# Optimization experiments

Hardware: AMD Instinct MI355X
Metric: run time of the kernel (lower is better)

The kernel has to match this reference:

```python
import jax, jax.numpy as jnp
import numpy as np

B, T, D = 4, 4096, 1024
EPS = 1e-5  # FusedRMSNormSwishGate default eps


def setup_inputs() -> dict:
    key = jax.random.key(0)
    ks = jax.random.split(key, 6)
    s = 1.0 / np.sqrt(D)
    return {
        "x": jax.random.normal(ks[0], (B, T, D), jnp.float32),
        "Wi": jax.random.normal(ks[1], (D, D), jnp.float32) * s,
        "Wf": jax.random.normal(ks[2], (D, D), jnp.float32) * s,
        "Wg": jax.random.normal(ks[3], (D, D), jnp.float32) * s,
        "Wo": jax.random.normal(ks[4], (D, D), jnp.float32) * s,
        "norm_w": jnp.ones((D,), jnp.float32),
    }


def _hgrn_scan(f, i):
    # h_t = f_t * h_{t-1} + i_t  (elementwise gated linear recurrence)
    # associative combine: (f1,i1) o (f2,i2) = (f1*f2, i1*f2 + i2)
    def combine(a, b):
        fa, ia = a
        fb, ib = b
        return fa * fb, ia * fb + ib

    _, h = jax.lax.associative_scan(combine, (f, i), axis=1)
    return h


def reference(x, Wi, Wf, Wg, Wo, norm_w):
    # projections
    i = x @ Wi.T                                  # [B,T,D]
    f = jax.nn.sigmoid(x @ Wf.T)                  # forget gate in (0,1)
    # swiglu(i, 1-f): silu on the value, gated by the input gate (1-f)
    inp = jax.nn.silu(i) * (1.0 - f)
    # hierarchically-gated linear recurrence (chunk/parallel scan form)
    h = _hgrn_scan(f, inp)                        # [B,T,D]
    # RMSNorm(h) * swish(g) output gate
    g = x @ Wg.T
    rms = h * jax.lax.rsqrt(jnp.mean(h * h, axis=-1, keepdims=True) + EPS)
    o = (rms * norm_w) * (g * jax.nn.sigmoid(g))
    return o @ Wo.T
```

## Files before the change

kernel.cpp:

```cpp
#include <hip/hip_runtime.h>
#include <hip/hip_bf16.h>

typedef unsigned short u16;
using bf16x8 = __bf16 __attribute__((ext_vector_type(8)));
using u16x8  = unsigned short __attribute__((ext_vector_type(8)));
using f32x4  = float  __attribute__((ext_vector_type(4)));

#define BB 4
#define TT 4096
#define DD 1024
#define MROWS (BB*TT)
#define CT 64
#define NC (TT/CT)

__device__ __forceinline__ float sigm(float x) { return 1.0f / (1.0f + __expf(-x)); }
__device__ __forceinline__ u16 f2bf(float f) {
    __hip_bfloat16 h = __float2bfloat16(f);
    return *reinterpret_cast<u16*>(&h);
}
__device__ __forceinline__ float bf2f(u16 u) { return __uint_as_float(((unsigned)u) << 16); }

__device__ __forceinline__ void async_cp16(const u16* g, u16* l) {
    __builtin_amdgcn_global_load_lds(
        (const __attribute__((address_space(1))) unsigned int*)g,
        (__attribute__((address_space(3))) unsigned int*)l, 16, 0, 0);
}

__global__ __launch_bounds__(256) void conv_w4_kernel(const float* __restrict__ w0,
                                                      const float* __restrict__ w1,
                                                      const float* __restrict__ w2,
                                                      const float* __restrict__ w3,
                                                      u16* __restrict__ dst) {
    int i = blockIdx.x * 256 + threadIdx.x;
    int sel = i >> 18;
    int off = i & 262143;
    const float* s = (sel == 0) ? w0 : (sel == 1) ? w1 : (sel == 2) ? w2 : w3;
    float4 v = *(const float4*)(s + (size_t)off * 4);
    ushort4 u;
    u.x = f2bf(v.x); u.y = f2bf(v.y); u.z = f2bf(v.z); u.w = f2bf(v.w);
    *(ushort4*)(dst + ((size_t)sel << 20) + (size_t)off * 4) = u;
}

#define BM 128
#define BN 128
#define BK 64

template <typename AT, typename OutT>
__global__ __launch_bounds__(256, 2)
void gemm_bt(const AT* __restrict__ Ag, const u16* __restrict__ Bg, int K,
             OutT* __restrict__ P0, OutT* __restrict__ P1, OutT* __restrict__ P2) {
    __shared__ u16 As[BM * BK];
    __shared__ u16 Bs[BN * BK];

    const int tid  = threadIdx.x;
    const int lane = tid & 63;
    const int wid  = tid >> 6;
    const int wm   = wid >> 1;
    const int wn   = wid & 1;
    const int lr   = lane & 15;
    const int lq   = lane >> 4;

    const long bM  = (long)blockIdx.y * BM;
    const long bN0 = (long)blockIdx.x * BN;

    const f32x4 zero = {0.f, 0.f, 0.f, 0.f};
    f32x4 acc[4][4];
#pragma unroll
    for (int i = 0; i < 4; i++)
#pragma unroll
        for (int j = 0; j < 4; j++) acc[i][j] = zero;

    for (int kt = 0; kt < K; kt += BK) {
        float4 afr[4][2];
        if constexpr (sizeof(AT) == 4) {
#pragma unroll
            for (int j = 0; j < 4; j++) {
                const int G  = j * 256 + tid;
                const int m  = G >> 3;
                const int gk = (G & 7) ^ (m & 7);
                const float* s = (const float*)Ag + (bM + m) * (long)K + kt + gk * 8;
                afr[j][0] = *(const float4*)s;
                afr[j][1] = *(const float4*)(s + 4);
            }
        }
        __syncthreads();
#pragma unroll
        for (int j = 0; j < 4; j++) {
            const int G  = j * 256 + tid;
            const int m  = G >> 3;
            const int gk = (G & 7) ^ (m & 7);
            if constexpr (sizeof(AT) == 4) {
                u16x8 wv;
                wv[0] = f2bf(afr[j][0].x); wv[1] = f2bf(afr[j][0].y);
                wv[2] = f2bf(afr[j][0].z); wv[3] = f2bf(afr[j][0].w);
                wv[4] = f2bf(afr[j][1].x); wv[5] = f2bf(afr[j][1].y);
                wv[6] = f2bf(afr[j][1].z); wv[7] = f2bf(afr[j][1].w);
                *(u16x8*)(&As[G * 8]) = wv;
            } else {
                async_cp16((const u16*)Ag + (bM + m) * (long)K + kt + gk * 8, &As[G * 8]);
            }
            async_cp16(Bg + (bN0 + m) * K + kt + gk * 8, &Bs[G * 8]);
        }
        __syncthreads();
#pragma unroll
        for (int kk = 0; kk < BK / 32; kk++) {
            bf16x8 av[4], bv[4];
#pragma unroll
            for (int f = 0; f < 4; f++) {
                const int am = wm * 64 + f * 16 + lr;
                const int ag = (kk * 4 + lq) ^ (am & 7);
                av[f] = *(const bf16x8*)(&As[am * 64 + ag * 8]);
                const int bn = wn * 64 + f * 16 + lr;
                const int bg = (kk * 4 + lq) ^ (bn & 7);
                bv[f] = *(const bf16x8*)(&Bs[bn * 64 + bg * 8]);
            }
#pragma unroll
            for (int i = 0; i < 4; i++)
#pragma unroll
                for (int j = 0; j < 4; j++)
                    acc[i][j] = __builtin_amdgcn_mfma_f32_16x16x32_bf16(av[i], bv[j],
                                                                        acc[i][j], 0, 0, 0);
        }
    }

    const int pl = (int)(bN0 >> 10);
    OutT* P = (pl == 0) ? P0 : ((pl == 1) ? P1 : P2);
    const int cn = (int)(bN0 & 1023);
#pragma unroll
    for (int i = 0; i < 4; i++) {
        const long m0 = bM + wm * 64 + i * 16 + lq * 4;
#pragma unroll
        for (int j = 0; j < 4; j++) {
            const int n = cn + wn * 64 + j * 16 + lr;
#pragma unroll
            for (int r = 0; r < 4; r++) {
                if constexpr (sizeof(OutT) == 2)
                    P[(m0 + r) * 1024 + n] = f2bf(acc[i][j][r]);
                else
                    P[(m0 + r) * 1024 + n] = acc[i][j][r];
            }
        }
    }
}

__global__ __launch_bounds__(256) void scan_pass1(const u16* __restrict__ ip,
                                                  const u16* __restrict__ fp,
                                                  float* __restrict__ Fc,
                                                  float* __restrict__ Ic) {
    const int tid = blockIdx.x * 256 + threadIdx.x;
    const int d4  = tid & 255;
    const int c   = (tid >> 8) & (NC - 1);
    const int b   = tid >> 14;
    size_t base = ((size_t)(b * TT + c * CT) << 10) + (size_t)d4 * 4;
    float F[4] = {1.f, 1.f, 1.f, 1.f};
    float I[4] = {0.f, 0.f, 0.f, 0.f};
#pragma unroll 8
    for (int t = 0; t < CT; t++) {
        ushort4 fu = *(const ushort4*)(fp + base);
        ushort4 iu = *(const ushort4*)(ip + base);
        base += DD;
        const u16 fa[4] = {fu.x, fu.y, fu.z, fu.w};
        const u16 ia[4] = {iu.x, iu.y, iu.z, iu.w};
#pragma unroll
        for (int j = 0; j < 4; j++) {
            float f  = sigm(bf2f(fa[j]));
            float iv = bf2f(ia[j]);
            float v  = iv * sigm(iv) * (1.f - f);
            I[j] = fmaf(f, I[j], v);
            F[j] *= f;
        }
    }
    const size_t o = (((size_t)(b * NC + c)) << 10) + (size_t)d4 * 4;
    float4 vF = {F[0], F[1], F[2], F[3]};
    float4 vI = {I[0], I[1], I[2], I[3]};
    *(float4*)(Fc + o) = vF;
    *(float4*)(Ic + o) = vI;
}

__global__ __launch_bounds__(256) void scan_pass2(const float* __restrict__ Fc,
                                                  const float* __restrict__ Ic,
                                                  float* __restrict__ Hin) {
    const int gtid = blockIdx.x * 256 + threadIdx.x;
    const int lane = gtid & 63;
    const int w    = gtid >> 6;
    const int b    = w >> 10;
    const int d    = w & 1023;
    const int idx  = ((b * NC + lane) << 10) + d;
    float F = Fc[idx];
    float I = Ic[idx];
#pragma unroll
    for (int s = 1; s < 64; s <<= 1) {
        float Fp = __shfl_up(F, s, 64);
        float Ip = __shfl_up(I, s, 64);
        if (lane >= s) {
            I = fmaf(Ip, F, I);
            F *= Fp;
        }
    }
    float Hex = __shfl_up(I, 1, 64);
    if (lane == 0) Hex = 0.f;
    Hin[idx] = Hex;
}

__global__ __launch_bounds__(256) void scan3_norm(const u16* __restrict__ ip,
                                                  const u16* __restrict__ fp,
                                                  const float* __restrict__ Hin,
                                                  const u16* __restrict__ gp,
                                                  const float* __restrict__ w,
                                                  u16* __restrict__ oout) {
    __shared__ u16 hlds[CT * DD];
    __shared__ float sw[4][CT];
    const int t_   = threadIdx.x;
    const int lane = t_ & 63;
    const int wv_  = t_ >> 6;
    const int c    = blockIdx.x & (NC - 1);
    const int b    = blockIdx.x >> 6;
    size_t base = ((size_t)(b * TT + c * CT) << 10) + (size_t)t_ * 4;
    const size_t o = (((size_t)(b * NC + c)) << 10) + (size_t)t_ * 4;
    float4 hv = *(const float4*)(Hin + o);
    float h[4] = {hv.x, hv.y, hv.z, hv.w};
    size_t rb = base;
#pragma unroll 4
    for (int t = 0; t < CT; t++) {
        ushort4 fu = *(const ushort4*)(fp + rb);
        ushort4 iu = *(const ushort4*)(ip + rb);
        rb += DD;
        const u16 fa[4] = {fu.x, fu.y, fu.z, fu.w};
        const u16 ia[4] = {iu.x, iu.y, iu.z, iu.w};
        float ss = 0.f;
        ushort4 hu;
        u16 ha[4];
#pragma unroll
        for (int j = 0; j < 4; j++) {
            float f  = sigm(bf2f(fa[j]));
            float iv = bf2f(ia[j]);
            float v  = iv * sigm(iv) * (1.f - f);
            h[j] = fmaf(f, h[j], v);
            ss = fmaf(h[j], h[j], ss);
            ha[j] = f2bf(h[j]);
        }
        hu.x = ha[0]; hu.y = ha[1]; hu.z = ha[2]; hu.w = ha[3];
        *(ushort4*)(&hlds[t * DD + t_ * 4]) = hu;
#pragma unroll
        for (int off = 32; off > 0; off >>= 1) ss += __shfl_down(ss, off);
        if (lane == 0) sw[wv_][t] = ss;
    }
    __syncthreads();
    const float4 wvv = *(const float4*)(w + (size_t)t_ * 4);
    const float wl[4] = {wvv.x, wvv.y, wvv.z, wvv.w};
    size_t wb = base;
#pragma unroll 4
    for (int t = 0; t < CT; t++) {
        const float tot = sw[0][t] + sw[1][t] + sw[2][t] + sw[3][t];
        const float rms = rsqrtf(tot * (1.f / 1024.f) + 1e-5f);
        ushort4 hu = *(const ushort4*)(&hlds[t * DD + t_ * 4]);
        ushort4 gu = *(const ushort4*)(gp + wb);
        const u16 ha[4] = {hu.x, hu.y, hu.z, hu.w};
        const u16 ga[4] = {gu.x, gu.y, gu.z, gu.w};
        ushort4 ou;
        u16 oa[4];
#pragma unroll
        for (int j = 0; j < 4; j++) {
            float gv = bf2f(ga[j]);
            oa[j] = f2bf(bf2f(ha[j]) * rms * wl[j] * gv * sigm(gv));
        }
        ou.x = oa[0]; ou.y = oa[1]; ou.z = oa[2]; ou.w = oa[3];
        *(ushort4*)(oout + wb) = ou;
        wb += DD;
    }
}

extern "C" void kernel_launch(void* const* d_in, const int* in_sizes, int n_in,
                              void* d_out, int out_size, void* d_ws, size_t ws_size,
                              hipStream_t stream) {
    const float* x  = (const float*)d_in[0];
    const float* Wi = (const float*)d_in[1];
    const float* Wf = (const float*)d_in[2];
    const float* Wg = (const float*)d_in[3];
    const float* Wo = (const float*)d_in[4];
    const float* nw = (const float*)d_in[5];
    float* out = (float*)d_out;

    const size_t MB = 1ull << 20;
    char* ws = (char*)d_ws;
    u16*   ob  = (u16*)(ws);
    u16*   Wb  = (u16*)(ws + 32 * MB);
    u16*   Pi  = (u16*)(ws + 40 * MB);
    u16*   Pf  = (u16*)(ws + 72 * MB);
    float* Fc  = (float*)(ws + 104 * MB);
    float* Ic  = Fc + BB * NC * DD;
    float* Hin = Ic + BB * NC * DD;
    u16*   g   = (u16*)d_out;

    conv_w4_kernel<<<4096, 256, 0, stream>>>(Wi, Wf, Wg, Wo, Wb);
    gemm_bt<float, u16><<<dim3(24, 128), 256, 0, stream>>>(x, Wb, 1024, Pi, Pf, g);
    scan_pass1<<<256, 256, 0, stream>>>(Pi, Pf, Fc, Ic);
    scan_pass2<<<1024, 256, 0, stream>>>(Fc, Ic, Hin);
    scan3_norm<<<256, 256, 0, stream>>>(Pi, Pf, Hin, g, nw, ob);
    gemm_bt<u16, float><<<dim3(8, 128), 256, 0, stream>>>(ob, Wb + 3ull * 1024 * 1024, 1024,
                                                          out, out, out);
}
```

Before: 415.9 us.

## Shrink scan chunks for more parallelism and async-load fp32 A tiles

Scan chunk length drops from 64 to 16, which quadruples the blocks for pass1 and scan3_norm. Pass2 now walks the chunk prefixes in segments of 64 with a carried state. Chunk state buffers move into the unused tail of the output buffer. The first GEMM now copies fp32 x tiles straight into LDS with async global_load_lds under an XOR swizzle, then converts them to bf16 after the LDS read, replacing the register-staged convert-then-store path. The aim is better occupancy in the scan kernels and removal of the register round trip for A, at the cost of twice the LDS for A and conversion work repeated by each wave.

```diff
diff --git a/kernel.cpp b/kernel.cpp
--- a/kernel.cpp
+++ b/kernel.cpp
@@ -3,14 +3,13 @@
 
 typedef unsigned short u16;
 using bf16x8 = __bf16 __attribute__((ext_vector_type(8)));
-using u16x8  = unsigned short __attribute__((ext_vector_type(8)));
 using f32x4  = float  __attribute__((ext_vector_type(4)));
 
 #define BB 4
 #define TT 4096
 #define DD 1024
 #define MROWS (BB*TT)
-#define CT 64
+#define CT 16
 #define NC (TT/CT)
 
 __device__ __forceinline__ float sigm(float x) { return 1.0f / (1.0f + __expf(-x)); }
@@ -49,8 +48,10 @@
 __global__ __launch_bounds__(256, 2)
 void gemm_bt(const AT* __restrict__ Ag, const u16* __restrict__ Bg, int K,
              OutT* __restrict__ P0, OutT* __restrict__ P1, OutT* __restrict__ P2) {
-    __shared__ u16 As[BM * BK];
+    __shared__ __align__(16) unsigned char AsRaw[BM * BK * sizeof(AT)];
     __shared__ u16 Bs[BN * BK];
+    u16*   As16 = (u16*)AsRaw;
+    float* As32 = (float*)AsRaw;
 
     const int tid  = threadIdx.x;
     const int lane = tid & 63;
@@ -71,34 +72,30 @@
         for (int j = 0; j < 4; j++) acc[i][j] = zero;
 
     for (int kt = 0; kt < K; kt += BK) {
-        float4 afr[4][2];
+        __syncthreads();
         if constexpr (sizeof(AT) == 4) {
+#pragma unroll
+            for (int j = 0; j < 8; j++) {
+                const int G  = j * 256 + tid;
+                const int m  = G >> 4;
+                const int gk = (G & 15) ^ (m & 15);
+                async_cp16((const u16*)((const float*)Ag + (bM + m) * (long)K + kt + gk * 4),
+                           (u16*)&As32[G * 4]);
+            }
+        } else {
 #pragma unroll
             for (int j = 0; j < 4; j++) {
                 const int G  = j * 256 + tid;
                 const int m  = G >> 3;
                 const int gk = (G & 7) ^ (m & 7);
-                const float* s = (const float*)Ag + (bM + m) * (long)K + kt + gk * 8;
-                afr[j][0] = *(const float4*)s;
-                afr[j][1] = *(const float4*)(s + 4);
-            }
-        }
-        __syncthreads();
+                async_cp16((const u16*)Ag + (bM + m) * (long)K + kt + gk * 8, &As16[G * 8]);
+            }
+        }
 #pragma unroll
         for (int j = 0; j < 4; j++) {
             const int G  = j * 256 + tid;
             const int m  = G >> 3;
             const int gk = (G & 7) ^ (m & 7);
-            if constexpr (sizeof(AT) == 4) {
-                u16x8 wv;
-                wv[0] = f2bf(afr[j][0].x); wv[1] = f2bf(afr[j][0].y);
-                wv[2] = f2bf(afr[j][0].z); wv[3] = f2bf(afr[j][0].w);
-                wv[4] = f2bf(afr[j][1].x); wv[5] = f2bf(afr[j][1].y);
-                wv[6] = f2bf(afr[j][1].z); wv[7] = f2bf(afr[j][1].w);
-                *(u16x8*)(&As[G * 8]) = wv;
-            } else {
-                async_cp16((const u16*)Ag + (bM + m) * (long)K + kt + gk * 8, &As[G * 8]);
-            }
             async_cp16(Bg + (bN0 + m) * K + kt + gk * 8, &Bs[G * 8]);
         }
         __syncthreads();
@@ -108,8 +105,22 @@
 #pragma unroll
             for (int f = 0; f < 4; f++) {
                 const int am = wm * 64 + f * 16 + lr;
-                const int ag = (kk * 4 + lq) ^ (am & 7);
-                av[f] = *(const bf16x8*)(&As[am * 64 + ag * 8]);
+                if constexpr (sizeof(AT) == 4) {
+                    const int g8 = kk * 4 + lq;
+                    const int pa = (2 * g8)     ^ (am & 15);
+                    const int pb = (2 * g8 + 1) ^ (am & 15);
+                    const f32x4 lo = *(const f32x4*)(&As32[am * 64 + pa * 4]);
+                    const f32x4 hi = *(const f32x4*)(&As32[am * 64 + pb * 4]);
+                    union { u16 s[8]; bf16x8 v; } u;
+                    u.s[0] = f2bf(lo[0]); u.s[1] = f2bf(lo[1]);
+                    u.s[2] = f2bf(lo[2]); u.s[3] = f2bf(lo[3]);
+                    u.s[4] = f2bf(hi[0]); u.s[5] = f2bf(hi[1]);
+                    u.s[6] = f2bf(hi[2]); u.s[7] = f2bf(hi[3]);
+                    av[f] = u.v;
+                } else {
+                    const int ag = (kk * 4 + lq) ^ (am & 7);
+                    av[f] = *(const bf16x8*)(&As16[am * 64 + ag * 8]);
+                }
                 const int bn = wn * 64 + f * 16 + lr;
                 const int bg = (kk * 4 + lq) ^ (bn & 7);
                 bv[f] = *(const bf16x8*)(&Bs[bn * 64 + bg * 8]);
@@ -150,11 +161,11 @@
     const int tid = blockIdx.x * 256 + threadIdx.x;
     const int d4  = tid & 255;
     const int c   = (tid >> 8) & (NC - 1);
-    const int b   = tid >> 14;
+    const int b   = tid >> 16;
     size_t base = ((size_t)(b * TT + c * CT) << 10) + (size_t)d4 * 4;
     float F[4] = {1.f, 1.f, 1.f, 1.f};
     float I[4] = {0.f, 0.f, 0.f, 0.f};
-#pragma unroll 8
+#pragma unroll
     for (int t = 0; t < CT; t++) {
         ushort4 fu = *(const ushort4*)(fp + base);
         ushort4 iu = *(const ushort4*)(ip + base);
@@ -185,21 +196,28 @@
     const int w    = gtid >> 6;
     const int b    = w >> 10;
     const int d    = w & 1023;
-    const int idx  = ((b * NC + lane) << 10) + d;
-    float F = Fc[idx];
-    float I = Ic[idx];
-#pragma unroll
-    for (int s = 1; s < 64; s <<= 1) {
-        float Fp = __shfl_up(F, s, 64);
-        float Ip = __shfl_up(I, s, 64);
-        if (lane >= s) {
-            I = fmaf(Ip, F, I);
-            F *= Fp;
-        }
-    }
-    float Hex = __shfl_up(I, 1, 64);
-    if (lane == 0) Hex = 0.f;
-    Hin[idx] = Hex;
+    float carryI = 0.f;
+#pragma unroll
+    for (int seg = 0; seg < NC / 64; seg++) {
+        const int c   = seg * 64 + lane;
+        const int idx = ((b * NC + c) << 10) + d;
+        float F = Fc[idx];
+        float I = Ic[idx];
+#pragma unroll
+        for (int s = 1; s < 64; s <<= 1) {
+            float Fp = __shfl_up(F, s, 64);
+            float Ip = __shfl_up(I, s, 64);
+            if (lane >= s) {
+                I = fmaf(Ip, F, I);
+                F *= Fp;
+            }
+        }
+        const float Itot = fmaf(carryI, F, I);
+        float Hex = __shfl_up(Itot, 1, 64);
+        if (lane == 0) Hex = carryI;
+        Hin[idx] = Hex;
+        carryI = __shfl(Itot, 63, 64);
+    }
 }
 
 __global__ __launch_bounds__(256) void scan3_norm(const u16* __restrict__ ip,
@@ -214,7 +232,7 @@
     const int lane = t_ & 63;
     const int wv_  = t_ >> 6;
     const int c    = blockIdx.x & (NC - 1);
-    const int b    = blockIdx.x >> 6;
+    const int b    = blockIdx.x >> 8;
     size_t base = ((size_t)(b * TT + c * CT) << 10) + (size_t)t_ * 4;
     const size_t o = (((size_t)(b * NC + c)) << 10) + (size_t)t_ * 4;
     float4 hv = *(const float4*)(Hin + o);
@@ -287,16 +305,16 @@
     u16*   Wb  = (u16*)(ws + 32 * MB);
     u16*   Pi  = (u16*)(ws + 40 * MB);
     u16*   Pf  = (u16*)(ws + 72 * MB);
-    float* Fc  = (float*)(ws + 104 * MB);
+    float* Fc  = (float*)((char*)d_out + 32 * MB);
     float* Ic  = Fc + BB * NC * DD;
     float* Hin = Ic + BB * NC * DD;
     u16*   g   = (u16*)d_out;
 
     conv_w4_kernel<<<4096, 256, 0, stream>>>(Wi, Wf, Wg, Wo, Wb);
     gemm_bt<float, u16><<<dim3(24, 128), 256, 0, stream>>>(x, Wb, 1024, Pi, Pf, g);
-    scan_pass1<<<256, 256, 0, stream>>>(Pi, Pf, Fc, Ic);
+    scan_pass1<<<1024, 256, 0, stream>>>(Pi, Pf, Fc, Ic);
     scan_pass2<<<1024, 256, 0, stream>>>(Fc, Ic, Hin);
-    scan3_norm<<<256, 256, 0, stream>>>(Pi, Pf, Hin, g, nw, ob);
+    scan3_norm<<<1024, 256, 0, stream>>>(Pi, Pf, Hin, g, nw, ob);
     gemm_bt<u16, float><<<dim3(8, 128), 256, 0, stream>>>(ob, Wb + 3ull * 1024 * 1024, 1024,
                                                           out, out, out);
 }
```

New measurement: 375.8 us. 9.7% less time.
